# Performance work log

Hardware: AMD Instinct MI355X
Metric: run time of the kernel (lower is better)

The kernel has to match this reference:

```python
import jax, jax.numpy as jnp
import numpy as np

CK, CV, CS = 8, 120, 64          # key / value / spatial-basis channels
NUM_AGENTS, NQ_PER = 4, 4        # queries chunked per agent; chunk(a,4) hard-codes NQ_PER=4
HID = 256                        # lstm_hidden_size
NA = 18                          # num_actions
U = 8                            # Fourier freqs; CS = U*U = 64
MLP_W = 512                      # q/a mlp hidden width


def spatial_basis(h, w):
    # fixed (h, w, CS) cos-product Fourier basis (SpatialBasis buffer)
    ph = jnp.arange(1, h + 1, dtype=jnp.float32)[:, None] * jnp.ones((1, w), jnp.float32) * (np.pi / h)
    pw = jnp.ones((h, 1), jnp.float32) * jnp.arange(1, w + 1, dtype=jnp.float32)[None, :] * (np.pi / w)
    u = jnp.arange(1, U + 1, dtype=jnp.float32)
    ca = jnp.cos(ph[..., None] * u)   # (h, w, U)
    cb = jnp.cos(pw[..., None] * u)   # (h, w, U)
    return jnp.einsum('hwu,hwv->hwuv', ca, cb).reshape(h, w, U * U)


def mlp3(x, w0, b0, w1, b1, w2, b2):
    # build_mlp with 2 relu hidden layers + identity output
    x = jax.nn.relu(x @ w0 + b0)
    x = jax.nn.relu(x @ w1 + b1)
    return x @ w2 + b2


def lstm_cell(x, h, c, w_ih, w_hh, b_ih, b_hh):
    gates = x @ w_ih.T + b_ih + h @ w_hh.T + b_hh
    i, f, g, o = jnp.split(gates, 4, axis=1)
    c2 = jax.nn.sigmoid(f) * c + jax.nn.sigmoid(i) * jnp.tanh(g)
    return jax.nn.sigmoid(o) * jnp.tanh(c2), c2


def setup_inputs() -> dict:
    key = jax.random.key(0)
    ks = jax.random.split(key, 24)
    n, h, w = 128, 64, 64
    s = 0.02
    nq = NUM_AGENTS * NQ_PER
    q_out = nq * (CK + CS)                       # 1152
    a_in = NQ_PER * (CK + 2 * CS + CV) + 2       # 1026
    r = lambda k, shp: jax.random.normal(k, shp, jnp.float32)
    return {
        'x': r(ks[0], (n, h, w, CK + CV)),
        'c': 1,
        'r_prev': r(ks[1], (n,)),
        'a_prev': r(ks[2], (n,)),
        'prev_hidden': r(ks[3], (n, HID)),
        'prev_cell': r(ks[4], (n, HID)),
        'q_w0': r(ks[5], (HID, MLP_W)) * s, 'q_b0': jnp.zeros((MLP_W,), jnp.float32),
        'q_w1': r(ks[6], (MLP_W, MLP_W)) * s, 'q_b1': jnp.zeros((MLP_W,), jnp.float32),
        'q_w2': r(ks[7], (MLP_W, q_out)) * s, 'q_b2': jnp.zeros((q_out,), jnp.float32),
        'a_w0': r(ks[8], (a_in, MLP_W)) * s, 'a_b0': jnp.zeros((MLP_W,), jnp.float32),
        'a_w1': r(ks[9], (MLP_W, MLP_W)) * s, 'a_b1': jnp.zeros((MLP_W,), jnp.float32),
        'a_w2': r(ks[10], (MLP_W, HID)) * s, 'a_b2': jnp.zeros((HID,), jnp.float32),
        'w_ih': r(ks[11], (4 * HID, HID)) * s, 'w_hh': r(ks[12], (4 * HID, HID)) * s,
        'b_ih': jnp.zeros((4 * HID,), jnp.float32), 'b_hh': jnp.zeros((4 * HID,), jnp.float32),
        'p_w': r(ks[13], (HID, NA)) * s, 'p_b': jnp.zeros((NA,), jnp.float32),
        'v_w': r(ks[14], (HID, NA)) * s, 'v_b': jnp.zeros((NA,), jnp.float32),
    }


def reference(x, c, r_prev, a_prev, prev_hidden, prev_cell,
              q_w0, q_b0, q_w1, q_b1, q_w2, q_b2,
              a_w0, a_b0, a_w1, a_b1, a_w2, a_b2,
              w_ih, w_hh, b_ih, b_hh, p_w, p_b, v_w, v_b):
    n, h, w, _ = x.shape
    S = spatial_basis(h, w)
    Sb = jnp.broadcast_to(S, (n, h, w, CS))
    K = jnp.concatenate([x[..., :CK], Sb], axis=-1)   # (n,h,w,CK+CS)
    V = jnp.concatenate([x[..., CK:], Sb], axis=-1)   # (n,h,w,CV+CS)
    # queries from previous hidden state, take agent c's chunk
    Q = mlp3(prev_hidden, q_w0, q_b0, q_w1, q_b1, q_w2, q_b2)
    Q = Q.reshape(n, NUM_AGENTS * NQ_PER, CK + CS)[:, c * NQ_PER:(c + 1) * NQ_PER, :]  # (n,4,CK+CS)
    # spatial QK attention with softmax over the h*w grid
    A = jnp.einsum('nhwd,nqd->nhwq', K, Q)            # (n,h,w,4)
    A = jax.nn.softmax(A.reshape(n, h * w, NQ_PER), axis=1).reshape(n, h, w, NQ_PER)
    a = jnp.einsum('nhwq,nhwd->nqd', A, V)            # (n,4,CV+CS)
    # concat answers + queries + prev reward/action scalars
    answer = jnp.concatenate([a.reshape(n, -1), Q.reshape(n, -1),
                              r_prev[:, None], a_prev[:, None]], axis=1)  # (n,1026)
    answer = mlp3(answer, a_w0, a_b0, a_w1, a_b1, a_w2, a_b2)             # (n,HID)
    hN, _cN = lstm_cell(answer, prev_hidden, prev_cell, w_ih, w_hh, b_ih, b_hh)
    logits = hN @ p_w + p_b
    values = hN @ v_w + v_b
    return logits, values
```

## Files before the change

kernel.cpp:

```cpp
#include <hip/hip_runtime.h>
#include <math.h>

#define NTOT   128
#define NPOS   4096
#define PVCH   16
#define PVLEN  256

__global__ __launch_bounds__(256) void k_gemm(
    const float* __restrict__ Ad, const float* __restrict__ pA,
    const float* __restrict__ biasA, int nzA, int reluA,
    const float* __restrict__ pvR,
    const float* __restrict__ W, float* __restrict__ pbuf,
    int N, int K, int ldw, int gkc, const int* __restrict__ cptr, int cmul) {
  __shared__ float Xs[4][128];
  const int t  = threadIdx.x;
  const int j  = blockIdx.x * 256 + t;
  const int m0 = blockIdx.y * 4;
  const int k0 = blockIdx.z * gkc;
  const int klen = min(gkc, K - k0);
  const int coff = cptr[0] * cmul;

  for (int idx = t; idx < 4 * klen; idx += 256) {
    int mi = idx / klen;
    int kk = idx - mi * klen;
    int col = k0 + kk;
    float s;
    if (Ad) {
      bool pv = false;
      int q = 0, d = 0;
      if (pvR && col < 736) {
        q = col / 184; d = col - q * 184;
        pv = (d < 120);
      }
      if (pv) {
        const size_t eo = (size_t)(m0 + mi) * 480 + q * 120 + d;
        float s0 = 0.f, s1 = 0.f, s2 = 0.f, s3 = 0.f;
#pragma unroll
        for (int c = 0; c < PVCH; c += 4) {
          s0 += pvR[(size_t)((c + 0) * NTOT) * 480 + eo];
          s1 += pvR[(size_t)((c + 1) * NTOT) * 480 + eo];
          s2 += pvR[(size_t)((c + 2) * NTOT) * 480 + eo];
          s3 += pvR[(size_t)((c + 3) * NTOT) * 480 + eo];
        }
        s = (s0 + s1) + (s2 + s3);
      } else {
        s = Ad[(size_t)(m0 + mi) * K + col];
      }
    } else {
      float s0 = biasA[col], s1 = 0.f, s2 = 0.f, s3 = 0.f;
      int z = 0;
      for (; z + 4 <= nzA; z += 4) {
        s0 += pA[((size_t)(z + 0) * NTOT + m0 + mi) * K + col];
        s1 += pA[((size_t)(z + 1) * NTOT + m0 + mi) * K + col];
        s2 += pA[((size_t)(z + 2) * NTOT + m0 + mi) * K + col];
        s3 += pA[((size_t)(z + 3) * NTOT + m0 + mi) * K + col];
      }
      for (; z < nzA; ++z) s0 += pA[((size_t)z * NTOT + m0 + mi) * K + col];
      s = (s0 + s1) + (s2 + s3);
      if (reluA) s = fmaxf(s, 0.f);
    }
    Xs[mi][kk] = s;
  }
  __syncthreads();

  if (j < N) {
    float acc[4];
#pragma unroll
    for (int mi = 0; mi < 4; ++mi) acc[mi] = 0.f;
    const float* wp = W + (size_t)k0 * ldw + coff + j;
#pragma unroll 16
    for (int kk = 0; kk < klen; ++kk) {
      float wv = wp[(size_t)kk * ldw];
#pragma unroll
      for (int mi = 0; mi < 4; ++mi) acc[mi] = fmaf(Xs[mi][kk], wv, acc[mi]);
    }
    float* op = pbuf + ((size_t)blockIdx.z * NTOT + m0) * N + j;
#pragma unroll
    for (int mi = 0; mi < 4; ++mi) op[(size_t)mi * N] = acc[mi];
  }
}

__global__ __launch_bounds__(1024) void k_logits(
    const float* __restrict__ x, const float* __restrict__ pQ,
    const float* __restrict__ q_b2, const int* __restrict__ cptr,
    const float* __restrict__ r_prev, const float* __restrict__ a_prev,
    float* __restrict__ Pw, float* __restrict__ ans) {
  const int n = blockIdx.x;
  const int t = threadIdx.x;
  const int wave = t >> 6, lane = t & 63;

  __shared__ float Qs[4][72];
  __shared__ float ct[64][8];
  __shared__ float cbQ[4 * 576];
  __shared__ float4 wlds[NPOS];
  __shared__ float red[4][16];
  __shared__ float mfin[4], lfin[4];
  __shared__ float rowSum[64][4][8];

  const float PI64 = 3.14159265358979323846f / 64.f;

  if (t < 288) {
    const int coff = cptr[0] * 288;
    float s = q_b2[coff + t];
#pragma unroll
    for (int z = 0; z < 8; ++z) s += pQ[((size_t)z * NTOT + n) * 288 + t];
    Qs[t / 72][t % 72] = s;
  }
  if (t < 512) {
    int i = t >> 3, u = t & 7;
    ct[i][u] = cosf((float)((i + 1) * (u + 1)) * PI64);
  }
  __syncthreads();

  for (int e = t; e < 2048; e += 1024) {
    int q = e >> 9, j = (e >> 3) & 63, u = e & 7;
    float s = 0.f;
#pragma unroll
    for (int v = 0; v < 8; ++v) s += ct[j][v] * Qs[q][8 + u * 8 + v];
    cbQ[q * 576 + j * 9 + u] = s;
  }
  __syncthreads();

  const float* xp = x + (size_t)n * NPOS * 128;
  float lmax[4] = {-1e30f, -1e30f, -1e30f, -1e30f};
#pragma unroll
  for (int r = 0; r < 4; ++r) {
    const int pos = r * 1024 + t;
    const int i = r * 16 + wave;
    const float4* xr = reinterpret_cast<const float4*>(xp + (size_t)pos * 128);
    float4 xa = xr[0], xb = xr[1];
    float lg[4];
#pragma unroll
    for (int q = 0; q < 4; ++q) {
      float s = xa.x * Qs[q][0] + xa.y * Qs[q][1] + xa.z * Qs[q][2] + xa.w * Qs[q][3]
              + xb.x * Qs[q][4] + xb.y * Qs[q][5] + xb.z * Qs[q][6] + xb.w * Qs[q][7];
      const float* cq = cbQ + q * 576 + lane * 9;
      float s2 = 0.f;
#pragma unroll
      for (int u = 0; u < 8; ++u) s2 += ct[i][u] * cq[u];
      lg[q] = s + s2;
      lmax[q] = fmaxf(lmax[q], lg[q]);
    }
    wlds[pos] = make_float4(lg[0], lg[1], lg[2], lg[3]);
  }

#pragma unroll
  for (int off = 32; off; off >>= 1)
#pragma unroll
    for (int q = 0; q < 4; ++q) lmax[q] = fmaxf(lmax[q], __shfl_xor(lmax[q], off));
  if (lane == 0)
#pragma unroll
    for (int q = 0; q < 4; ++q) red[q][wave] = lmax[q];
  __syncthreads();
  if (t < 4) {
    float m = red[t][0];
#pragma unroll
    for (int w = 1; w < 16; ++w) m = fmaxf(m, red[t][w]);
    mfin[t] = m;
  }
  __syncthreads();

  float lsum[4] = {0.f, 0.f, 0.f, 0.f};
#pragma unroll
  for (int r = 0; r < 4; ++r) {
    const int pos = r * 1024 + t;
    float4 w = wlds[pos];
    w.x = __expf(w.x - mfin[0]);
    w.y = __expf(w.y - mfin[1]);
    w.z = __expf(w.z - mfin[2]);
    w.w = __expf(w.w - mfin[3]);
    wlds[pos] = w;
    lsum[0] += w.x; lsum[1] += w.y; lsum[2] += w.z; lsum[3] += w.w;
  }
#pragma unroll
  for (int off = 32; off; off >>= 1)
#pragma unroll
    for (int q = 0; q < 4; ++q) lsum[q] += __shfl_xor(lsum[q], off);
  if (lane == 0)
#pragma unroll
    for (int q = 0; q < 4; ++q) red[q][wave] = lsum[q];
  __syncthreads();
  if (t < 4) {
    float s = 0.f;
#pragma unroll
    for (int w = 0; w < 16; ++w) s += red[t][w];
    lfin[t] = s;
  }
  __syncthreads();

  const float i0 = 1.f / lfin[0], i1 = 1.f / lfin[1];
  const float i2 = 1.f / lfin[2], i3 = 1.f / lfin[3];

  float4* Pw4 = reinterpret_cast<float4*>(Pw) + (size_t)n * NPOS;
#pragma unroll
  for (int r = 0; r < 4; ++r) {
    const int pos = r * 1024 + t;
    float4 w = wlds[pos];
    Pw4[pos] = make_float4(w.x * i0, w.y * i1, w.z * i2, w.w * i3);
  }

  for (int o = t; o < 2048; o += 1024) {
    int i = o >> 5, q = (o >> 3) & 3, v = o & 7;
    float s0 = 0.f, s1 = 0.f, s2 = 0.f, s3 = 0.f;
    const float* wb = reinterpret_cast<const float*>(&wlds[i * 64]) + q;
#pragma unroll 8
    for (int j = 0; j < 64; j += 4) {
      s0 += wb[(j + 0) * 4] * ct[j + 0][v];
      s1 += wb[(j + 1) * 4] * ct[j + 1][v];
      s2 += wb[(j + 2) * 4] * ct[j + 2][v];
      s3 += wb[(j + 3) * 4] * ct[j + 3][v];
    }
    float inv = (q == 0) ? i0 : (q == 1) ? i1 : (q == 2) ? i2 : i3;
    rowSum[i][q][v] = ((s0 + s1) + (s2 + s3)) * inv;
  }
  __syncthreads();

  float* ap = ans + (size_t)n * 1026;
  if (t < 256) {
    int q = t >> 6, uv = t & 63, u = uv >> 3, v = uv & 7;
    float s = 0.f;
#pragma unroll 8
    for (int i = 0; i < 64; ++i) s += ct[i][u] * rowSum[i][q][v];
    ap[q * 184 + 120 + uv] = s;
  } else if (t < 544) {
    int qi = t - 256;
    ap[736 + qi] = Qs[qi / 72][qi % 72];
  } else if (t == 544) {
    ap[1024] = r_prev[n];
  } else if (t == 545) {
    ap[1025] = a_prev[n];
  }
}

__global__ __launch_bounds__(256, 4) void k_pv(
    const float* __restrict__ x, const float* __restrict__ Pw,
    float* __restrict__ pvp) {
  const int n = blockIdx.y, ck = blockIdx.x;
  const int t = threadIdx.x, wave = t >> 6, lane = t & 63;
  __shared__ float4 wl[PVLEN];
  __shared__ __align__(16) float part[4][4][120];

  const int base = ck * PVLEN;
  wl[t] = reinterpret_cast<const float4*>(Pw)[(size_t)n * NPOS + base + t];
  __syncthreads();

  const int xl = (lane < 60) ? lane : 59;
  const float* vb = x + ((size_t)n * NPOS + base + wave * 64) * 128 + 8 + 2 * xl;

  float ax0[4] = {0.f, 0.f, 0.f, 0.f};
  float ax1[4] = {0.f, 0.f, 0.f, 0.f};
#pragma unroll
  for (int b = 0; b < 4; ++b) {
    float2 v0  = *reinterpret_cast<const float2*>(vb + (size_t)(b * 16 + 0)  * 128);
    float2 v1  = *reinterpret_cast<const float2*>(vb + (size_t)(b * 16 + 1)  * 128);
    float2 v2  = *reinterpret_cast<const float2*>(vb + (size_t)(b * 16 + 2)  * 128);
    float2 v3  = *reinterpret_cast<const float2*>(vb + (size_t)(b * 16 + 3)  * 128);
    float2 v4  = *reinterpret_cast<const float2*>(vb + (size_t)(b * 16 + 4)  * 128);
    float2 v5  = *reinterpret_cast<const float2*>(vb + (size_t)(b * 16 + 5)  * 128);
    float2 v6  = *reinterpret_cast<const float2*>(vb + (size_t)(b * 16 + 6)  * 128);
    float2 v7  = *reinterpret_cast<const float2*>(vb + (size_t)(b * 16 + 7)  * 128);
    float2 v8  = *reinterpret_cast<const float2*>(vb + (size_t)(b * 16 + 8)  * 128);
    float2 v9  = *reinterpret_cast<const float2*>(vb + (size_t)(b * 16 + 9)  * 128);
    float2 v10 = *reinterpret_cast<const float2*>(vb + (size_t)(b * 16 + 10) * 128);
    float2 v11 = *reinterpret_cast<const float2*>(vb + (size_t)(b * 16 + 11) * 128);
    float2 v12 = *reinterpret_cast<const float2*>(vb + (size_t)(b * 16 + 12) * 128);
    float2 v13 = *reinterpret_cast<const float2*>(vb + (size_t)(b * 16 + 13) * 128);
    float2 v14 = *reinterpret_cast<const float2*>(vb + (size_t)(b * 16 + 14) * 128);
    float2 v15 = *reinterpret_cast<const float2*>(vb + (size_t)(b * 16 + 15) * 128);
#define ACC(VV, II)                                                              \
    {                                                                            \
      float4 w = wl[wave * 64 + b * 16 + II];                                    \
      ax0[0] += w.x * VV.x; ax1[0] += w.x * VV.y;                                \
      ax0[1] += w.y * VV.x; ax1[1] += w.y * VV.y;                                \
      ax0[2] += w.z * VV.x; ax1[2] += w.z * VV.y;                                \
      ax0[3] += w.w * VV.x; ax1[3] += w.w * VV.y;                                \
    }
    ACC(v0, 0)  ACC(v1, 1)  ACC(v2, 2)  ACC(v3, 3)
    ACC(v4, 4)  ACC(v5, 5)  ACC(v6, 6)  ACC(v7, 7)
    ACC(v8, 8)  ACC(v9, 9)  ACC(v10, 10) ACC(v11, 11)
    ACC(v12, 12) ACC(v13, 13) ACC(v14, 14) ACC(v15, 15)
#undef ACC
  }
  if (lane < 60) {
#pragma unroll
    for (int q = 0; q < 4; ++q)
      *reinterpret_cast<float2*>(&part[wave][q][2 * lane]) = make_float2(ax0[q], ax1[q]);
  }
  __syncthreads();

  float* op = pvp + ((size_t)ck * NTOT + n) * 480;
  for (int idx = t; idx < 480; idx += 256) {
    const int q = idx / 120, d = idx - q * 120;
    op[idx] = (part[0][q][d] + part[1][q][d]) + (part[2][q][d] + part[3][q][d]);
  }
}

__global__ __launch_bounds__(256) void k_gates(
    const float* __restrict__ pA, const float* __restrict__ biasA,
    const float* __restrict__ hp,
    const float* __restrict__ w_ih, const float* __restrict__ w_hh,
    const float* __restrict__ b_ih, const float* __restrict__ b_hh,
    float* __restrict__ gbuf) {
  const int t = threadIdx.x;
  const int n0 = blockIdx.x * 2;
  const int r0 = blockIdx.y * 64;
  __shared__ float xs[2][256], hs[2][256];
  __shared__ float red[64][4][5];
#pragma unroll
  for (int s = 0; s < 2; ++s) {
    float v0 = biasA[t], v1 = 0.f, v2 = 0.f, v3 = 0.f;
#pragma unroll
    for (int z = 0; z < 8; z += 4) {
      v0 += pA[((size_t)(z + 0) * NTOT + n0 + s) * 256 + t];
      v1 += pA[((size_t)(z + 1) * NTOT + n0 + s) * 256 + t];
      v2 += pA[((size_t)(z + 2) * NTOT + n0 + s) * 256 + t];
      v3 += pA[((size_t)(z + 3) * NTOT + n0 + s) * 256 + t];
    }
    xs[s][t] = (v0 + v1) + (v2 + v3);
    hs[s][t] = hp[(size_t)(n0 + s) * 256 + t];
  }
  __syncthreads();
  const int r = t >> 2, kq = t & 3;
  const int row = r0 + r;
  const float4* wi = reinterpret_cast<const float4*>(w_ih + (size_t)row * 256 + kq * 64);
  const float4* wh = reinterpret_cast<const float4*>(w_hh + (size_t)row * 256 + kq * 64);
  float s00 = 0.f, s01 = 0.f, s10 = 0.f, s11 = 0.f;
#pragma unroll
  for (int i = 0; i < 16; ++i) {
    float4 a = wi[i], b = wh[i];
    const int k4 = kq * 64 + i * 4;
    s00 += a.x * xs[0][k4] + a.y * xs[0][k4 + 1] + a.z * xs[0][k4 + 2] + a.w * xs[0][k4 + 3];
    s01 += a.x * xs[1][k4] + a.y * xs[1][k4 + 1] + a.z * xs[1][k4 + 2] + a.w * xs[1][k4 + 3];
    s10 += b.x * hs[0][k4] + b.y * hs[0][k4 + 1] + b.z * hs[0][k4 + 2] + b.w * hs[0][k4 + 3];
    s11 += b.x * hs[1][k4] + b.y * hs[1][k4 + 1] + b.z * hs[1][k4 + 2] + b.w * hs[1][k4 + 3];
  }
  red[r][kq][0] = s00; red[r][kq][1] = s01; red[r][kq][2] = s10; red[r][kq][3] = s11;
  __syncthreads();
  if (t < 128) {
    const int rr = t >> 1, s = t & 1;
    float g = b_ih[r0 + rr] + b_hh[r0 + rr];
#pragma unroll
    for (int k = 0; k < 4; ++k) g += red[rr][k][s] + red[rr][k][2 + s];
    gbuf[(size_t)(n0 + s) * 1024 + r0 + rr] = g;
  }
}

__global__ __launch_bounds__(256) void k_lstm2(
    const float* __restrict__ gbuf, const float* __restrict__ cp,
    const float* __restrict__ p_w, const float* __restrict__ p_b,
    const float* __restrict__ v_w, const float* __restrict__ v_b,
    float* __restrict__ out) {
  const int t = threadIdx.x;
  const int n0 = blockIdx.x * 2;
  __shared__ float h2[2][256];
#pragma unroll
  for (int s = 0; s < 2; ++s) {
    const size_t gb = (size_t)(n0 + s) * 1024;
    float gi = gbuf[gb + t], gf = gbuf[gb + 256 + t];
    float gg = gbuf[gb + 512 + t], go = gbuf[gb + 768 + t];
    float si = 1.f / (1.f + __expf(-gi));
    float sf = 1.f / (1.f + __expf(-gf));
    float so = 1.f / (1.f + __expf(-go));
    float c2 = sf * cp[(size_t)(n0 + s) * 256 + t] + si * tanhf(gg);
    h2[s][t] = so * tanhf(c2);
  }
  __syncthreads();
  if (t < 72) {
    const int si = t / 36, r = t % 36, iv = r / 18, j = r % 18;
    const float* W = iv ? v_w : p_w;
    const float* B = iv ? v_b : p_b;
    float s = B[j];
#pragma unroll 8
    for (int k = 0; k < 256; ++k) s += h2[si][k] * W[k * 18 + j];
    out[(size_t)iv * (NTOT * 18) + (size_t)(n0 + si) * 18 + j] = s;
  }
}

extern "C" void kernel_launch(void* const* d_in, const int* in_sizes, int n_in,
                              void* d_out, int out_size, void* d_ws, size_t ws_size,
                              hipStream_t stream) {
  const float* x      = (const float*)d_in[0];
  const int*   cptr   = (const int*)d_in[1];
  const float* r_prev = (const float*)d_in[2];
  const float* a_prev = (const float*)d_in[3];
  const float* hprev  = (const float*)d_in[4];
  const float* cprev  = (const float*)d_in[5];
  const float* q_w0 = (const float*)d_in[6];
  const float* q_b0 = (const float*)d_in[7];
  const float* q_w1 = (const float*)d_in[8];
  const float* q_b1 = (const float*)d_in[9];
  const float* q_w2 = (const float*)d_in[10];
  const float* q_b2 = (const float*)d_in[11];
  const float* a_w0 = (const float*)d_in[12];
  const float* a_b0 = (const float*)d_in[13];
  const float* a_w1 = (const float*)d_in[14];
  const float* a_b1 = (const float*)d_in[15];
  const float* a_w2 = (const float*)d_in[16];
  const float* a_b2 = (const float*)d_in[17];
  const float* w_ih = (const float*)d_in[18];
  const float* w_hh = (const float*)d_in[19];
  const float* b_ih = (const float*)d_in[20];
  const float* b_hh = (const float*)d_in[21];
  const float* p_w  = (const float*)d_in[22];
  const float* p_b  = (const float*)d_in[23];
  const float* v_w  = (const float*)d_in[24];
  const float* v_b  = (const float*)d_in[25];
  float* out = (float*)d_out;
  float* ws  = (float*)d_ws;

  float* pQ  = ws;
  float* pb1 = pQ  + 294912;
  float* pb2 = pb1 + 589824;
  float* pb3 = pb2 + 524288;
  float* Pw  = pb3 + 262144;
  float* pvp = Pw  + 2097152;
  float* ans = pvp + 983040;
  float* gbuf= ans + 131328;

  k_gemm<<<dim3(2, 32, 4), 256, 0, stream>>>(hprev, nullptr, nullptr, 0, 0, nullptr,
                                             q_w0, pb1, 512, 256, 512, 64, cptr, 0);
  k_gemm<<<dim3(2, 32, 8), 256, 0, stream>>>(nullptr, pb1, q_b0, 4, 1, nullptr,
                                             q_w1, pb2, 512, 512, 512, 64, cptr, 0);
  k_gemm<<<dim3(2, 32, 8), 256, 0, stream>>>(nullptr, pb2, q_b1, 8, 1, nullptr,
                                             q_w2, pQ, 288, 512, 1152, 64, cptr, 288);

  k_logits<<<NTOT, 1024, 0, stream>>>(x, pQ, q_b2, cptr, r_prev, a_prev, Pw, ans);
  k_pv<<<dim3(PVCH, NTOT), 256, 0, stream>>>(x, Pw, pvp);

  k_gemm<<<dim3(2, 32, 9), 256, 0, stream>>>(ans, nullptr, nullptr, 0, 0, pvp,
                                             a_w0, pb1, 512, 1026, 512, 128, cptr, 0);
  k_gemm<<<dim3(2, 32, 8), 256, 0, stream>>>(nullptr, pb1, a_b0, 9, 1, nullptr,
                                             a_w1, pb2, 512, 512, 512, 64, cptr, 0);
  k_gemm<<<dim3(1, 32, 8), 256, 0, stream>>>(nullptr, pb2, a_b1, 8, 1, nullptr,
                                             a_w2, pb3, 256, 512, 256, 64, cptr, 0);

  k_gates<<<dim3(64, 16), 256, 0, stream>>>(pb3, a_b2, hprev, w_ih, w_hh, b_ih, b_hh, gbuf);
  k_lstm2<<<64, 256, 0, stream>>>(gbuf, cprev, p_w, p_b, v_w, v_b, out);
}
```

Baseline: 136.5 us.

## Split logits kernel across spatial chunks and defer softmax normalization downstream

```diff
diff --git a/kernel.cpp b/kernel.cpp
--- a/kernel.cpp
+++ b/kernel.cpp
@@ -5,11 +5,13 @@
 #define NPOS   4096
 #define PVCH   16
 #define PVLEN  256
+#define LCH    8
+#define LCLEN  512
 
 __global__ __launch_bounds__(256) void k_gemm(
     const float* __restrict__ Ad, const float* __restrict__ pA,
     const float* __restrict__ biasA, int nzA, int reluA,
-    const float* __restrict__ pvR,
+    const float* __restrict__ pvR, const float* __restrict__ scl,
     const float* __restrict__ W, float* __restrict__ pbuf,
     int N, int K, int ldw, int gkc, const int* __restrict__ cptr, int cmul) {
   __shared__ float Xs[4][128];
@@ -42,7 +44,7 @@
           s2 += pvR[(size_t)((c + 2) * NTOT) * 480 + eo];
           s3 += pvR[(size_t)((c + 3) * NTOT) * 480 + eo];
         }
-        s = (s0 + s1) + (s2 + s3);
+        s = ((s0 + s1) + (s2 + s3)) * scl[(size_t)(m0 + mi) * 4 + q];
       } else {
         s = Ad[(size_t)(m0 + mi) * K + col];
       }
@@ -80,22 +82,22 @@
   }
 }
 
-__global__ __launch_bounds__(1024) void k_logits(
+__global__ __launch_bounds__(512) void k_logits(
     const float* __restrict__ x, const float* __restrict__ pQ,
     const float* __restrict__ q_b2, const int* __restrict__ cptr,
     const float* __restrict__ r_prev, const float* __restrict__ a_prev,
-    float* __restrict__ Pw, float* __restrict__ ans) {
-  const int n = blockIdx.x;
-  const int t = threadIdx.x;
+    float* __restrict__ Pw, float* __restrict__ Lpart,
+    float* __restrict__ rsum, float* __restrict__ ans) {
+  const int ck = blockIdx.x;
+  const int n  = blockIdx.y;
+  const int t  = threadIdx.x;
   const int wave = t >> 6, lane = t & 63;
 
   __shared__ float Qs[4][72];
   __shared__ float ct[64][8];
   __shared__ float cbQ[4 * 576];
-  __shared__ float4 wlds[NPOS];
-  __shared__ float red[4][16];
-  __shared__ float mfin[4], lfin[4];
-  __shared__ float rowSum[64][4][8];
+  __shared__ float4 wlds[LCLEN];
+  __shared__ float red[4][8];
 
   const float PI64 = 3.14159265358979323846f / 64.f;
 
@@ -106,13 +108,13 @@
     for (int z = 0; z < 8; ++z) s += pQ[((size_t)z * NTOT + n) * 288 + t];
     Qs[t / 72][t % 72] = s;
   }
-  if (t < 512) {
+  {
     int i = t >> 3, u = t & 7;
     ct[i][u] = cosf((float)((i + 1) * (u + 1)) * PI64);
   }
   __syncthreads();
 
-  for (int e = t; e < 2048; e += 1024) {
+  for (int e = t; e < 2048; e += 512) {
     int q = e >> 9, j = (e >> 3) & 63, u = e & 7;
     float s = 0.f;
 #pragma unroll
@@ -121,14 +123,15 @@
   }
   __syncthreads();
 
+  const int base = ck * LCLEN;
   const float* xp = x + (size_t)n * NPOS * 128;
-  float lmax[4] = {-1e30f, -1e30f, -1e30f, -1e30f};
-#pragma unroll
-  for (int r = 0; r < 4; ++r) {
-    const int pos = r * 1024 + t;
-    const int i = r * 16 + wave;
+
+  const int irow = ck * 8 + wave;
+  {
+    const int pos = base + t;
     const float4* xr = reinterpret_cast<const float4*>(xp + (size_t)pos * 128);
     float4 xa = xr[0], xb = xr[1];
+    float4 w;
     float lg[4];
 #pragma unroll
     for (int q = 0; q < 4; ++q) {
@@ -137,72 +140,35 @@
       const float* cq = cbQ + q * 576 + lane * 9;
       float s2 = 0.f;
 #pragma unroll
-      for (int u = 0; u < 8; ++u) s2 += ct[i][u] * cq[u];
+      for (int u = 0; u < 8; ++u) s2 += ct[irow][u] * cq[u];
       lg[q] = s + s2;
-      lmax[q] = fmaxf(lmax[q], lg[q]);
-    }
-    wlds[pos] = make_float4(lg[0], lg[1], lg[2], lg[3]);
-  }
-
-#pragma unroll
-  for (int off = 32; off; off >>= 1)
-#pragma unroll
-    for (int q = 0; q < 4; ++q) lmax[q] = fmaxf(lmax[q], __shfl_xor(lmax[q], off));
-  if (lane == 0)
-#pragma unroll
-    for (int q = 0; q < 4; ++q) red[q][wave] = lmax[q];
-  __syncthreads();
-  if (t < 4) {
-    float m = red[t][0];
-#pragma unroll
-    for (int w = 1; w < 16; ++w) m = fmaxf(m, red[t][w]);
-    mfin[t] = m;
-  }
-  __syncthreads();
-
-  float lsum[4] = {0.f, 0.f, 0.f, 0.f};
-#pragma unroll
-  for (int r = 0; r < 4; ++r) {
-    const int pos = r * 1024 + t;
-    float4 w = wlds[pos];
-    w.x = __expf(w.x - mfin[0]);
-    w.y = __expf(w.y - mfin[1]);
-    w.z = __expf(w.z - mfin[2]);
-    w.w = __expf(w.w - mfin[3]);
-    wlds[pos] = w;
-    lsum[0] += w.x; lsum[1] += w.y; lsum[2] += w.z; lsum[3] += w.w;
-  }
-#pragma unroll
-  for (int off = 32; off; off >>= 1)
-#pragma unroll
-    for (int q = 0; q < 4; ++q) lsum[q] += __shfl_xor(lsum[q], off);
-  if (lane == 0)
-#pragma unroll
-    for (int q = 0; q < 4; ++q) red[q][wave] = lsum[q];
+    }
+    w.x = __expf(lg[0]); w.y = __expf(lg[1]);
+    w.z = __expf(lg[2]); w.w = __expf(lg[3]);
+    wlds[t] = w;
+    reinterpret_cast<float4*>(Pw)[(size_t)n * NPOS + base + t] = w;
+
+    float lsum[4] = {w.x, w.y, w.z, w.w};
+#pragma unroll
+    for (int off = 32; off; off >>= 1)
+#pragma unroll
+      for (int q = 0; q < 4; ++q) lsum[q] += __shfl_xor(lsum[q], off);
+    if (lane == 0)
+#pragma unroll
+      for (int q = 0; q < 4; ++q) red[q][wave] = lsum[q];
+  }
   __syncthreads();
   if (t < 4) {
     float s = 0.f;
 #pragma unroll
-    for (int w = 0; w < 16; ++w) s += red[t][w];
-    lfin[t] = s;
-  }
-  __syncthreads();
-
-  const float i0 = 1.f / lfin[0], i1 = 1.f / lfin[1];
-  const float i2 = 1.f / lfin[2], i3 = 1.f / lfin[3];
-
-  float4* Pw4 = reinterpret_cast<float4*>(Pw) + (size_t)n * NPOS;
-#pragma unroll
-  for (int r = 0; r < 4; ++r) {
-    const int pos = r * 1024 + t;
-    float4 w = wlds[pos];
-    Pw4[pos] = make_float4(w.x * i0, w.y * i1, w.z * i2, w.w * i3);
-  }
-
-  for (int o = t; o < 2048; o += 1024) {
-    int i = o >> 5, q = (o >> 3) & 3, v = o & 7;
+    for (int w8 = 0; w8 < 8; ++w8) s += red[t][w8];
+    Lpart[((size_t)n * LCH + ck) * 4 + t] = s;
+  }
+
+  if (t < 256) {
+    int i = t >> 5, q = (t >> 3) & 3, v = t & 7;
+    const float* wb = reinterpret_cast<const float*>(&wlds[i * 64]) + q;
     float s0 = 0.f, s1 = 0.f, s2 = 0.f, s3 = 0.f;
-    const float* wb = reinterpret_cast<const float*>(&wlds[i * 64]) + q;
 #pragma unroll 8
     for (int j = 0; j < 64; j += 4) {
       s0 += wb[(j + 0) * 4] * ct[j + 0][v];
@@ -210,35 +176,26 @@
       s2 += wb[(j + 2) * 4] * ct[j + 2][v];
       s3 += wb[(j + 3) * 4] * ct[j + 3][v];
     }
-    float inv = (q == 0) ? i0 : (q == 1) ? i1 : (q == 2) ? i2 : i3;
-    rowSum[i][q][v] = ((s0 + s1) + (s2 + s3)) * inv;
-  }
-  __syncthreads();
-
-  float* ap = ans + (size_t)n * 1026;
-  if (t < 256) {
-    int q = t >> 6, uv = t & 63, u = uv >> 3, v = uv & 7;
-    float s = 0.f;
-#pragma unroll 8
-    for (int i = 0; i < 64; ++i) s += ct[i][u] * rowSum[i][q][v];
-    ap[q * 184 + 120 + uv] = s;
-  } else if (t < 544) {
-    int qi = t - 256;
-    ap[736 + qi] = Qs[qi / 72][qi % 72];
-  } else if (t == 544) {
-    ap[1024] = r_prev[n];
-  } else if (t == 545) {
-    ap[1025] = a_prev[n];
+    rsum[((size_t)n * 64 + ck * 8 + i) * 32 + q * 8 + v] = (s0 + s1) + (s2 + s3);
+  }
+
+  if (ck == 0) {
+    float* ap = ans + (size_t)n * 1026;
+    if (t < 288) ap[736 + t] = Qs[t / 72][t % 72];
+    if (t == 288) { ap[1024] = r_prev[n]; ap[1025] = a_prev[n]; }
   }
 }
 
 __global__ __launch_bounds__(256, 4) void k_pv(
     const float* __restrict__ x, const float* __restrict__ Pw,
-    float* __restrict__ pvp) {
+    const float* __restrict__ Lpart, const float* __restrict__ rsum,
+    float* __restrict__ pvp, float* __restrict__ scl, float* __restrict__ ans) {
   const int n = blockIdx.y, ck = blockIdx.x;
   const int t = threadIdx.x, wave = t >> 6, lane = t & 63;
   __shared__ float4 wl[PVLEN];
   __shared__ __align__(16) float part[4][4][120];
+  __shared__ float ct2[64][8];
+  __shared__ float sc_s[4];
 
   const int base = ck * PVLEN;
   wl[t] = reinterpret_cast<const float4*>(Pw)[(size_t)n * NPOS + base + t];
@@ -292,6 +249,36 @@
   for (int idx = t; idx < 480; idx += 256) {
     const int q = idx / 120, d = idx - q * 120;
     op[idx] = (part[0][q][d] + part[1][q][d]) + (part[2][q][d] + part[3][q][d]);
+  }
+
+  if (ck == 0) {
+    const float PI64 = 3.14159265358979323846f / 64.f;
+    if (t < 4) {
+      float L = 0.f;
+#pragma unroll
+      for (int c = 0; c < LCH; ++c) L += Lpart[((size_t)n * LCH + c) * 4 + t];
+      float s = 1.f / L;
+      scl[(size_t)n * 4 + t] = s;
+      sc_s[t] = s;
+    }
+    for (int e = t; e < 512; e += 256) {
+      int i = e >> 3, u = e & 7;
+      ct2[i][u] = cosf((float)((i + 1) * (u + 1)) * PI64);
+    }
+    __syncthreads();
+    {
+      const int q = t >> 6, uv = t & 63, u = uv >> 3, v = uv & 7;
+      const float* rp = rsum + (size_t)n * 64 * 32 + q * 8 + v;
+      float s0 = 0.f, s1 = 0.f, s2 = 0.f, s3 = 0.f;
+#pragma unroll 8
+      for (int row = 0; row < 64; row += 4) {
+        s0 += ct2[row + 0][u] * rp[(row + 0) * 32];
+        s1 += ct2[row + 1][u] * rp[(row + 1) * 32];
+        s2 += ct2[row + 2][u] * rp[(row + 2) * 32];
+        s3 += ct2[row + 3][u] * rp[(row + 3) * 32];
+      }
+      ans[(size_t)n * 1026 + q * 184 + 120 + uv] = sc_s[q] * ((s0 + s1) + (s2 + s3));
+    }
   }
 }
 
@@ -408,30 +395,34 @@
   float* out = (float*)d_out;
   float* ws  = (float*)d_ws;
 
-  float* pQ  = ws;
-  float* pb1 = pQ  + 294912;
-  float* pb2 = pb1 + 589824;
-  float* pb3 = pb2 + 524288;
-  float* Pw  = pb3 + 262144;
-  float* pvp = Pw  + 2097152;
-  float* ans = pvp + 983040;
-  float* gbuf= ans + 131328;
-
-  k_gemm<<<dim3(2, 32, 4), 256, 0, stream>>>(hprev, nullptr, nullptr, 0, 0, nullptr,
+  float* pQ   = ws;
+  float* pb1  = pQ   + 294912;
+  float* pb2  = pb1  + 589824;
+  float* pb3  = pb2  + 524288;
+  float* Pw   = pb3  + 262144;
+  float* pvp  = Pw   + 2097152;
+  float* ans  = pvp  + 983040;
+  float* gbuf = ans  + 131328;
+  float* Lp   = gbuf + 131072;
+  float* rsum = Lp   + 4096;
+  float* scl  = rsum + 262144;
+
+  k_gemm<<<dim3(2, 32, 4), 256, 0, stream>>>(hprev, nullptr, nullptr, 0, 0, nullptr, nullptr,
                                              q_w0, pb1, 512, 256, 512, 64, cptr, 0);
-  k_gemm<<<dim3(2, 32, 8), 256, 0, stream>>>(nullptr, pb1, q_b0, 4, 1, nullptr,
+  k_gemm<<<dim3(2, 32, 8), 256, 0, stream>>>(nullptr, pb1, q_b0, 4, 1, nullptr, nullptr,
                                              q_w1, pb2, 512, 512, 512, 64, cptr, 0);
-  k_gemm<<<dim3(2, 32, 8), 256, 0, stream>>>(nullptr, pb2, q_b1, 8, 1, nullptr,
+  k_gemm<<<dim3(2, 32, 8), 256, 0, stream>>>(nullptr, pb2, q_b1, 8, 1, nullptr, nullptr,
                                              q_w2, pQ, 288, 512, 1152, 64, cptr, 288);
 
-  k_logits<<<NTOT, 1024, 0, stream>>>(x, pQ, q_b2, cptr, r_prev, a_prev, Pw, ans);
-  k_pv<<<dim3(PVCH, NTOT), 256, 0, stream>>>(x, Pw, pvp);
-
-  k_gemm<<<dim3(2, 32, 9), 256, 0, stream>>>(ans, nullptr, nullptr, 0, 0, pvp,
+  k_logits<<<dim3(LCH, NTOT), 512, 0, stream>>>(x, pQ, q_b2, cptr, r_prev, a_prev,
+                                                Pw, Lp, rsum, ans);
+  k_pv<<<dim3(PVCH, NTOT), 256, 0, stream>>>(x, Pw, Lp, rsum, pvp, scl, ans);
+
+  k_gemm<<<dim3(2, 32, 9), 256, 0, stream>>>(ans, nullptr, nullptr, 0, 0, pvp, scl,
                                              a_w0, pb1, 512, 1026, 512, 128, cptr, 0);
-  k_gemm<<<dim3(2, 32, 8), 256, 0, stream>>>(nullptr, pb1, a_b0, 9, 1, nullptr,
+  k_gemm<<<dim3(2, 32, 8), 256, 0, stream>>>(nullptr, pb1, a_b0, 9, 1, nullptr, nullptr,
                                              a_w1, pb2, 512, 512, 512, 64, cptr, 0);
-  k_gemm<<<dim3(1, 32, 8), 256, 0, stream>>>(nullptr, pb2, a_b1, 8, 1, nullptr,
+  k_gemm<<<dim3(1, 32, 8), 256, 0, stream>>>(nullptr, pb2, a_b1, 8, 1, nullptr, nullptr,
                                              a_w2, pb3, 256, 512, 256, 64, cptr, 0);
 
   k_gates<<<dim3(64, 16), 256, 0, stream>>>(pb3, a_b2, hprev, w_ih, w_hh, b_ih, b_hh, gbuf);
```

Measured after the change: 133.4 us, median of 2. 1.02x faster.
